# Kernel tuning notes

Measured on AMD Instinct MI355X. Metric: run time of the kernel, lower is better.

The kernel has to match this reference:

```python
import jax, jax.numpy as jnp
import numpy as np

# Static module hyperparameters (init_kwargs)
P = 3        # num_partitions
C = 1024     # channels
V = 64       # num_joints
F = 512      # fifo_size
K = 9        # kernel_size (temporal sum width)
D = 63       # stride -> dilation of conv3d_sum


def setup_inputs() -> dict:
    key = jax.random.key(0)
    k1, k2, k3 = jax.random.split(key, 3)
    x = jax.random.normal(k1, (1, P * C, 1, V), dtype=jnp.float32)
    graph = jax.random.uniform(k2, (P, V, V), dtype=jnp.float32)      # adjacency A (P,V,V)
    fifo = jax.random.normal(k3, (1, 1, C, F, V), dtype=jnp.float32)  # FIFO state
    return {"x": x, "graph": graph, "fifo": fifo}


def reference(x, graph, fifo):
    # x.unfold(dim=1, size=C, step=C): (1, P*C, 1, V) -> (1, P, 1, V, C)
    x5 = x.reshape(1, P, C, 1, V).transpose(0, 1, 3, 4, 2)  # (1,P,1,V,C)
    # conv3d_matmul with weight[j,p,0,u,0] = A[p,u,j] (graph adjacency matmul):
    # out[n,j,t,c] = sum_{p,u} A[p,u,j] * x5[n,p,t,u,c]
    y = jnp.einsum('nptuc,puj->njtc', x5, graph)            # (1,V,1,C)
    # permute(0,2,4,3,1): (N,J,T,1,C) -> (N,T,C,1,J)
    x_perm = y.transpose(0, 2, 3, 1)[:, :, :, None, :]      # (1,1,C,1,V)
    # FIFO shift: push newest frame, drop oldest
    new_fifo = jnp.concatenate([x_perm, fifo[:, :, :, :-1]], axis=3)  # (1,1,C,F,V)
    # conv3d_sum: all-ones (1,K,1) kernel with temporal dilation D
    Hout = F - D * (K - 1)  # = 8
    out = new_fifo[:, :, :, 0:Hout, :]
    for i in range(1, K):
        out = out + new_fifo[:, :, :, i * D:i * D + Hout, :]
    return out[:, 0]  # (1, C, Hout, V)
```

## Files before the change

kernel.cpp:

```cpp
#include <hip/hip_runtime.h>


#define P 3
#define C 1024
#define V 64
#define F 512
#define K 9
#define D 63
#define HOUT 8

__global__ __launch_bounds__(512) void stgcn_kernel(
    const float* __restrict__ x,
    const float* __restrict__ graph,
    const float* __restrict__ fifo,
    float* __restrict__ out)
{
    const int c = blockIdx.x;
    const int t = threadIdx.x;
    const int h = t >> 6;
    const int v = t & 63;

    __shared__ float xs[P * V];

    if (t < P * V) {
        const int p = t >> 6;
        const int u = t & 63;
        xs[t] = x[(p * C + c) * V + u];
    }
    __syncthreads();

    float acc;
    if (h == 0) {
        float s = 0.f;
        #pragma unroll
        for (int pu = 0; pu < P * V; ++pu) {
            s = fmaf(xs[pu], graph[pu * V + v], s);
        }
        acc = s;
    } else {
        acc = fifo[(c * F + (h - 1)) * V + v];
    }

    const float* frow = fifo + (size_t)c * F * V + (size_t)(h - 1) * V + v;
    #pragma unroll
    for (int i = 1; i < K; ++i) {
        acc += frow[(size_t)i * D * V];
    }

    out[(c * HOUT + h) * V + v] = acc;
}

extern "C" void kernel_launch(void* const* d_in, const int* in_sizes, int n_in,
                              void* d_out, int out_size, void* d_ws, size_t ws_size,
                              hipStream_t stream) {
    const float* x     = (const float*)d_in[0];
    const float* graph = (const float*)d_in[1];
    const float* fifo  = (const float*)d_in[2];
    float* out = (float*)d_out;

    stgcn_kernel<<<C, 512, 0, stream>>>(x, graph, fifo, out);
}
```

Before: 9.932 us.

## Vectorize with float4 and split graph matmul across all rows with shared reduction

Reduces the block to 128 threads, each handling four consecutive joints with float4 loads and stores. The 192-term graph matmul that one wavefront did alone is now split across all 8 row groups, with partial sums reduced through shared memory. All fifo taps are issued before the barrier so their latency overlaps the matmul. The cost is an extra barrier, more registers for buffered taps, and a partial read of tap rows at h=0 that the reduction ignores.

```diff
diff --git a/kernel.cpp b/kernel.cpp
--- a/kernel.cpp
+++ b/kernel.cpp
@@ -9,54 +9,81 @@
 #define D 63
 #define HOUT 8
 
-__global__ __launch_bounds__(512) void stgcn_kernel(
+__global__ __launch_bounds__(128) void stgcn_kernel(
     const float* __restrict__ x,
-    const float* __restrict__ graph,
-    const float* __restrict__ fifo,
-    float* __restrict__ out)
+    const float4* __restrict__ g4,
+    const float4* __restrict__ fifo4,
+    float4* __restrict__ out4)
 {
     const int c = blockIdx.x;
     const int t = threadIdx.x;
-    const int h = t >> 6;
-    const int v = t & 63;
+    const int h = t >> 4;
+    const int q = t & 15;
 
-    __shared__ float xs[P * V];
+    __shared__ float  xs[P * V];
+    __shared__ float4 part[8][16];
 
-    if (t < P * V) {
-        const int p = t >> 6;
-        const int u = t & 63;
-        xs[t] = x[(p * C + c) * V + u];
+    for (int idx = t; idx < P * V; idx += 128) {
+        xs[idx] = x[((idx >> 6) * C + c) * V + (idx & 63)];
     }
     __syncthreads();
 
-    float acc;
-    if (h == 0) {
-        float s = 0.f;
-        #pragma unroll
-        for (int pu = 0; pu < P * V; ++pu) {
-            s = fmaf(xs[pu], graph[pu * V + v], s);
-        }
-        acc = s;
-    } else {
-        acc = fifo[(c * F + (h - 1)) * V + v];
+    float ax = 0.f, ay = 0.f, az = 0.f, aw = 0.f;
+    const int pu0 = h * 24;
+    #pragma unroll
+    for (int i = 0; i < 24; ++i) {
+        const int pu = pu0 + i;
+        const float  xv = xs[pu];
+        const float4 gg = g4[pu * 16 + q];
+        ax = fmaf(xv, gg.x, ax);
+        ay = fmaf(xv, gg.y, ay);
+        az = fmaf(xv, gg.z, az);
+        aw = fmaf(xv, gg.w, aw);
+    }
+    part[h][q] = make_float4(ax, ay, az, aw);
+
+    const long base = (long)c * (F * 16) + (long)(h - 1) * 16 + q;
+    float rx, ry, rz, rw;
+    float4 f0;
+    if (h > 0) {
+        f0 = fifo4[base];
     }
 
-    const float* frow = fifo + (size_t)c * F * V + (size_t)(h - 1) * V + v;
+    float4 tap[K - 1];
     #pragma unroll
     for (int i = 1; i < K; ++i) {
-        acc += frow[(size_t)i * D * V];
+        tap[i - 1] = fifo4[base + (long)i * (D * 16)];
     }
 
-    out[(c * HOUT + h) * V + v] = acc;
+    __syncthreads();
+
+    if (h == 0) {
+        float4 s = part[0][q];
+        rx = s.x; ry = s.y; rz = s.z; rw = s.w;
+        #pragma unroll
+        for (int g = 1; g < 8; ++g) {
+            float4 pgq = part[g][q];
+            rx += pgq.x; ry += pgq.y; rz += pgq.z; rw += pgq.w;
+        }
+    } else {
+        rx = f0.x; ry = f0.y; rz = f0.z; rw = f0.w;
+    }
+
+    #pragma unroll
+    for (int i = 0; i < K - 1; ++i) {
+        rx += tap[i].x; ry += tap[i].y; rz += tap[i].z; rw += tap[i].w;
+    }
+
+    out4[(c * HOUT + h) * 16 + q] = make_float4(rx, ry, rz, rw);
 }
 
 extern "C" void kernel_launch(void* const* d_in, const int* in_sizes, int n_in,
                               void* d_out, int out_size, void* d_ws, size_t ws_size,
                               hipStream_t stream) {
-    const float* x     = (const float*)d_in[0];
-    const float* graph = (const float*)d_in[1];
-    const float* fifo  = (const float*)d_in[2];
-    float* out = (float*)d_out;
+    const float*  x     = (const float*)d_in[0];
+    const float4* graph = (const float4*)d_in[1];
+    const float4* fifo  = (const float4*)d_in[2];
+    float4* out = (float4*)d_out;
 
-    stgcn_kernel<<<C, 512, 0, stream>>>(x, graph, fifo, out);
+    stgcn_kernel<<<C, 128, 0, stream>>>(x, graph, fifo, out);
 }
```

Result: no change. 9.785 us (-1.5%).
